# Kernel optimization log

Hardware: AMD Instinct MI355X
Metric: run time of the kernel (lower is better)

The kernel has to match this reference:

```python
import jax, jax.numpy as jnp
import numpy as np

D = 1024
F = 256
EPS = 1e-5


def layer_norm(x, g, b):
    mu = jnp.mean(x, axis=-1, keepdims=True)
    var = jnp.mean((x - mu) ** 2, axis=-1, keepdims=True)
    return (x - mu) * jax.lax.rsqrt(var + EPS) * g + b


def setup_inputs() -> dict:
    key = jax.random.key(0)
    ks = jax.random.split(key, 8)
    B, S = 4, 4096
    return {
        "bottom_up_input": jax.random.normal(ks[0], (B, S, D), dtype=jnp.float32),
        "top_down_prediction": jax.random.normal(ks[1], (B, S, D), dtype=jnp.float32),
        "W_spec": jax.random.normal(ks[2], (2 * F, D), dtype=jnp.float32) * 0.02,
        "log_decay": jnp.linspace(-3.0, -0.001, F, dtype=jnp.float32),
        "frequencies": jax.random.normal(ks[3], (F,), dtype=jnp.float32) * 0.1,
        "W_from": jax.random.normal(ks[4], (D, 2 * F), dtype=jnp.float32) * 0.02,
        "ln1_g": jnp.ones((D,), jnp.float32),
        "ln1_b": jnp.zeros((D,), jnp.float32),
        "W1": jax.random.normal(ks[5], (D, D), dtype=jnp.float32) * 0.02,
        "b1": jnp.zeros((D,), jnp.float32),
        "W2": jax.random.normal(ks[6], (D, D), dtype=jnp.float32) * 0.02,
        "b2": jnp.zeros((D,), jnp.float32),
        "ln2_g": jnp.ones((D,), jnp.float32),
        "ln2_b": jnp.zeros((D,), jnp.float32),
        "error_weight": jnp.asarray(0.1, jnp.float32),
    }


def spectral_conv(x, W_spec, log_decay, frequencies, W_from, ln1_g, ln1_b):
    # x: [B,S,D]
    x = layer_norm(x, ln1_g, ln1_b)
    B, S, _ = x.shape
    spectral = jnp.einsum('bsd,fd->bsf', x, W_spec)  # [B,S,2F]
    u = jax.lax.complex(spectral[..., :F], spectral[..., F:])  # [B,S,F] complex
    decay = jax.nn.sigmoid(log_decay)
    omega = jnp.tanh(frequencies) * 0.1  # dt = 1.0
    rot = jax.lax.complex(jnp.cos(omega), jnp.sin(omega))  # [F]
    A = (decay * rot).astype(jnp.complex64)  # [F]
    # kernel[t] = A^t * rot, built with cumprod as in the original
    ones = jnp.ones((1, F), dtype=A.dtype)
    A_seq = jnp.broadcast_to(A[None, :], (S - 1, F))
    powers = jnp.cumprod(jnp.concatenate([ones, A_seq], axis=0), axis=0)  # [S,F]
    kernel = (powers * rot[None, :])[None]  # [1,S,F]
    n_fft = 2 * S
    U_f = jnp.fft.fft(u, n=n_fft, axis=1)
    K_f = jnp.fft.fft(kernel, n=n_fft, axis=1)
    y = jnp.fft.ifft(U_f * K_f, n=n_fft, axis=1)[:, :S, :]  # [B,S,F]
    spectral_out = jnp.concatenate([y.real, y.imag], axis=-1)  # [B,S,2F]
    return jnp.einsum('bsf,df->bsd', spectral_out, W_from)


def reference(bottom_up_input, top_down_prediction, W_spec, log_decay, frequencies,
              W_from, ln1_g, ln1_b, W1, b1, W2, b2, ln2_g, ln2_b, error_weight):
    bu_repr = spectral_conv(bottom_up_input, W_spec, log_decay, frequencies,
                            W_from, ln1_g, ln1_b)
    error = jnp.clip(bu_repr - top_down_prediction, -1.0, 1.0)
    corrected = bu_repr - jax.nn.sigmoid(error_weight) * error
    prediction_error = jnp.clip(jnp.mean(error ** 2), 0.0, 1.0)
    h = jax.nn.gelu(jnp.einsum('bsd,ed->bse', corrected, W1) + b1, approximate=False)
    h = jnp.einsum('bsd,ed->bse', h, W2) + b2
    next_prediction = layer_norm(h, ln2_g, ln2_b)
    return corrected, next_prediction, prediction_error
```

## Files before the change

kernel.cpp:

```cpp
#include <hip/hip_runtime.h>
#include <math.h>

#define Dn 1024
#define Fn 256
#define Sn 4096
#define Bn 4
#define Mn (Bn*Sn)
#define CHn 256
#define NCn (Sn/CHn)

typedef __bf16 bf16x8 __attribute__((ext_vector_type(8)));
typedef float  f32x4  __attribute__((ext_vector_type(4)));

__device__ inline unsigned short f2bf(float f) {
  unsigned int u = __float_as_uint(f);
  u += 0x7fffu + ((u >> 16) & 1u);
  return (unsigned short)(u >> 16);
}
__device__ inline float bf2f(unsigned short s) {
  return __uint_as_float(((unsigned int)s) << 16);
}

__device__ inline void async16(const void* g, void* l) {
  __builtin_amdgcn_global_load_lds(
      (__attribute__((address_space(1))) void*)(g),
      (__attribute__((address_space(3))) void*)(l), 16, 0, 0);
}

#define WAITVM(n) __builtin_amdgcn_s_waitcnt(0xF70 | (n))
#define BARRIER() asm volatile("s_barrier" ::: "memory")

__global__ __launch_bounds__(256) void convert_weights(
    const float* __restrict__ wspec, const float* __restrict__ wfrom,
    const float* __restrict__ w1, const float* __restrict__ w2,
    unsigned short* __restrict__ o_spec, unsigned short* __restrict__ o_from,
    unsigned short* __restrict__ o_w1, unsigned short* __restrict__ o_w2) {
  int i = blockIdx.x * 256 + threadIdx.x;
  if (i < 524288) {
    o_spec[i] = f2bf(wspec[i]);
    o_from[i] = f2bf(wfrom[i]);
  }
  o_w1[i] = f2bf(w1[i]);
  o_w2[i] = f2bf(w2[i]);
}

template <int OUT_BF16>
__global__ __launch_bounds__(256) void ln_kernel(
    const float* __restrict__ x, const float* __restrict__ g,
    const float* __restrict__ b, void* __restrict__ out) {
  int row = blockIdx.x, tid = threadIdx.x;
  int wid = tid >> 6, lane = tid & 63;
  float4 v = ((const float4*)(x + (size_t)row * Dn))[tid];
  float s  = v.x + v.y + v.z + v.w;
  float ss = v.x * v.x + v.y * v.y + v.z * v.z + v.w * v.w;
  #pragma unroll
  for (int o = 32; o; o >>= 1) {
    s  += __shfl_down(s, o);
    ss += __shfl_down(ss, o);
  }
  __shared__ float r1[4], r2[4];
  if (lane == 0) { r1[wid] = s; r2[wid] = ss; }
  __syncthreads();
  s  = r1[0] + r1[1] + r1[2] + r1[3];
  ss = r2[0] + r2[1] + r2[2] + r2[3];
  float mu  = s * (1.0f / Dn);
  float var = ss * (1.0f / Dn) - mu * mu;
  float rs  = rsqrtf(var + 1e-5f);
  float4 gv = ((const float4*)g)[tid];
  float4 bv = ((const float4*)b)[tid];
  float o0 = (v.x - mu) * rs * gv.x + bv.x;
  float o1 = (v.y - mu) * rs * gv.y + bv.y;
  float o2 = (v.z - mu) * rs * gv.z + bv.z;
  float o3 = (v.w - mu) * rs * gv.w + bv.w;
  if (OUT_BF16) {
    ushort4 w;
    w.x = f2bf(o0); w.y = f2bf(o1); w.z = f2bf(o2); w.w = f2bf(o3);
    ((ushort4*)out)[(size_t)row * 256 + tid] = w;
  } else {
    float4 w; w.x = o0; w.y = o1; w.z = o2; w.w = o3;
    ((float4*)out)[(size_t)row * 256 + tid] = w;
  }
}

template <int MODE>
__global__ __launch_bounds__(256) void gemm_bt(
    const unsigned short* __restrict__ A, const unsigned short* __restrict__ Bw,
    int K, int N,
    float* __restrict__ outF, unsigned short* __restrict__ outH,
    const float* __restrict__ td, const float* __restrict__ bias,
    const float* __restrict__ ew, float* __restrict__ errAcc) {
  __shared__ unsigned short As[3 * 4096];
  __shared__ unsigned short Bs[3 * 4096];
  __shared__ float red[4];

  int tid = threadIdx.x;
  int wid = tid >> 6, lane = tid & 63;
  int wm = wid >> 1, wn = wid & 1;
  int quad = lane >> 4, l16 = lane & 15;

  int g = blockIdx.x + gridDim.x * blockIdx.y;
  int nbn = gridDim.x;
  int gh = g >> 3;
  int bn = gh % nbn;
  int bm = (g & 7) + (gh / nbn) * 8;

  int r_lo = lane >> 2;
  int c8   = (lane & 3) * 8;

  const unsigned short* Abase = A + (size_t)bm * 128 * K;
  const unsigned short* Bbase = Bw + (size_t)bn * 128 * K;

  f32x4 acc[4][4] = {};

  const int T = K >> 5;
  auto issue = [&](int t, int stg) {
    int k0 = t << 5;
    #pragma unroll
    for (int s = 0; s < 2; ++s) {
      int chunk = s * 4 + wid;
      int r = chunk * 16 + r_lo;
      async16(Abase + (size_t)r * K + k0 + c8, As + stg * 4096 + chunk * 512);
      async16(Bbase + (size_t)r * K + k0 + c8, Bs + stg * 4096 + chunk * 512);
    }
  };

  issue(0, 0);
  if (T > 1) issue(1, 1);

  int stg = 0, stg2 = 2;
  for (int k = 0; k < T; ++k) {
    if (k + 1 < T) WAITVM(4); else WAITVM(0);
    BARRIER();
    if (k + 2 < T) issue(k + 2, stg2);

    const unsigned short* Ab = As + stg * 4096;
    const unsigned short* Bb = Bs + stg * 4096;
    bf16x8 af[4], bf[4];
    #pragma unroll
    for (int i = 0; i < 4; i++)
      af[i] = *(const bf16x8*)(Ab + (wm * 64 + i * 16 + l16) * 32 + quad * 8);
    #pragma unroll
    for (int j = 0; j < 4; j++)
      bf[j] = *(const bf16x8*)(Bb + (wn * 64 + j * 16 + l16) * 32 + quad * 8);
    #pragma unroll
    for (int i = 0; i < 4; i++)
      #pragma unroll
      for (int j = 0; j < 4; j++)
        acc[i][j] = __builtin_amdgcn_mfma_f32_16x16x32_bf16(af[i], bf[j], acc[i][j], 0, 0, 0);

    stg  = (stg  == 2) ? 0 : stg  + 1;
    stg2 = (stg2 == 2) ? 0 : stg2 + 1;
  }

  float esum = 0.0f;
  float sigw = 0.0f;
  if (MODE == 1) sigw = 1.0f / (1.0f + expf(-ew[0]));

  #pragma unroll
  for (int i = 0; i < 4; i++) {
    int row_base = bm * 128 + wm * 64 + i * 16 + quad * 4;
    #pragma unroll
    for (int j = 0; j < 4; j++) {
      int col = bn * 128 + wn * 64 + j * 16 + l16;
      #pragma unroll
      for (int r = 0; r < 4; r++) {
        size_t idx = (size_t)(row_base + r) * N + col;
        float v = acc[i][j][r];
        if (MODE == 0) {
          outH[idx] = f2bf(v);
        } else if (MODE == 1) {
          float e = v - td[idx];
          e = fminf(fmaxf(e, -1.0f), 1.0f);
          float corr = v - sigw * e;
          outF[idx] = corr;
          outH[idx] = f2bf(corr);
          esum += e * e;
        } else if (MODE == 2) {
          float h = v + bias[col];
          float gel = 0.5f * h * (1.0f + erff(h * 0.70710678118654752f));
          outH[idx] = f2bf(gel);
        } else {
          outF[idx] = v + bias[col];
        }
      }
    }
  }

  if (MODE == 1) {
    #pragma unroll
    for (int o = 32; o; o >>= 1) esum += __shfl_down(esum, o);
    if (lane == 0) red[wid] = esum;
    __syncthreads();
    if (tid == 0) atomicAdd(errAcc, red[0] + red[1] + red[2] + red[3]);
  }
}

__global__ __launch_bounds__(256) void scan_partial(
    const unsigned short* __restrict__ spec, const float* __restrict__ log_decay,
    const float* __restrict__ freq, float2* __restrict__ chunkfin) {
  int f = threadIdx.x;
  int bx = blockIdx.x;
  int b = bx / NCn, c = bx % NCn;
  float dec = 1.0f / (1.0f + expf(-log_decay[f]));
  float om  = tanhf(freq[f]) * 0.1f;
  float Are = dec * cosf(om), Aim = dec * sinf(om);
  const unsigned short* u = spec + ((size_t)b * Sn + (size_t)c * CHn) * 512 + f;
  float sre = 0.0f, sim = 0.0f;
  for (int t = 0; t < CHn; t++) {
    float ure = bf2f(u[(size_t)t * 512]);
    float uim = bf2f(u[(size_t)t * 512 + 256]);
    float nre = Are * sre - Aim * sim + ure;
    float nim = Are * sim + Aim * sre + uim;
    sre = nre; sim = nim;
  }
  chunkfin[(size_t)bx * 256 + f] = make_float2(sre, sim);
}

__global__ __launch_bounds__(256) void scan_carry(
    const float* __restrict__ log_decay, const float* __restrict__ freq,
    const float2* __restrict__ chunkfin, float2* __restrict__ carries) {
  int f = threadIdx.x;
  int b = blockIdx.x;
  float dec = 1.0f / (1.0f + expf(-log_decay[f]));
  float om  = tanhf(freq[f]) * 0.1f;
  float pre = dec * cosf(om), pim = dec * sinf(om);
  #pragma unroll
  for (int i = 0; i < 8; i++) {
    float nr = pre * pre - pim * pim;
    float ni = 2.0f * pre * pim;
    pre = nr; pim = ni;
  }
  float sre = 0.0f, sim = 0.0f;
  for (int c = 0; c < NCn; c++) {
    carries[(size_t)(b * NCn + c) * 256 + f] = make_float2(sre, sim);
    float2 cf = chunkfin[(size_t)(b * NCn + c) * 256 + f];
    float nre = pre * sre - pim * sim + cf.x;
    float nim = pre * sim + pim * sre + cf.y;
    sre = nre; sim = nim;
  }
}

__global__ __launch_bounds__(256) void scan_final(
    const unsigned short* __restrict__ spec, const float* __restrict__ log_decay,
    const float* __restrict__ freq, const float2* __restrict__ carries,
    unsigned short* __restrict__ outH) {
  int f = threadIdx.x;
  int bx = blockIdx.x;
  int b = bx / NCn, c = bx % NCn;
  float dec = 1.0f / (1.0f + expf(-log_decay[f]));
  float om  = tanhf(freq[f]) * 0.1f;
  float Are = dec * cosf(om), Aim = dec * sinf(om);
  float Rre = cosf(om), Rim = sinf(om);
  float2 s0 = carries[(size_t)bx * 256 + f];
  float sre = s0.x, sim = s0.y;
  const unsigned short* u = spec + ((size_t)b * Sn + (size_t)c * CHn) * 512 + f;
  unsigned short* o = outH + ((size_t)b * Sn + (size_t)c * CHn) * 512 + f;
  for (int t = 0; t < CHn; t++) {
    float ure = bf2f(u[(size_t)t * 512]);
    float uim = bf2f(u[(size_t)t * 512 + 256]);
    float nre = Are * sre - Aim * sim + ure;
    float nim = Are * sim + Aim * sre + uim;
    sre = nre; sim = nim;
    o[(size_t)t * 512]       = f2bf(Rre * sre - Rim * sim);
    o[(size_t)t * 512 + 256] = f2bf(Rre * sim + Rim * sre);
  }
}

__global__ void finalize_err(const float* __restrict__ errAcc, float* __restrict__ out) {
  float m = errAcc[0] * (1.0f / 16777216.0f);
  out[0] = fminf(fmaxf(m, 0.0f), 1.0f);
}

extern "C" void kernel_launch(void* const* d_in, const int* in_sizes, int n_in,
                              void* d_out, int out_size, void* d_ws, size_t ws_size,
                              hipStream_t stream) {
  (void)in_sizes; (void)n_in; (void)out_size; (void)ws_size;
  const float* x     = (const float*)d_in[0];
  const float* td    = (const float*)d_in[1];
  const float* wspec = (const float*)d_in[2];
  const float* logd  = (const float*)d_in[3];
  const float* freq  = (const float*)d_in[4];
  const float* wfrom = (const float*)d_in[5];
  const float* g1    = (const float*)d_in[6];
  const float* b1ln  = (const float*)d_in[7];
  const float* W1    = (const float*)d_in[8];
  const float* b1    = (const float*)d_in[9];
  const float* W2    = (const float*)d_in[10];
  const float* b2    = (const float*)d_in[11];
  const float* g2    = (const float*)d_in[12];
  const float* b2ln  = (const float*)d_in[13];
  const float* ew    = (const float*)d_in[14];

  char* ws = (char*)d_ws;
  size_t off = 0;
  float* errAcc = (float*)(ws + off);              off += 256;
  unsigned short* wspec_h = (unsigned short*)(ws + off); off += (size_t)512 * 1024 * 2;
  unsigned short* wfrom_h = (unsigned short*)(ws + off); off += (size_t)1024 * 512 * 2;
  unsigned short* w1_h    = (unsigned short*)(ws + off); off += (size_t)1024 * 1024 * 2;
  unsigned short* w2_h    = (unsigned short*)(ws + off); off += (size_t)1024 * 1024 * 2;
  unsigned short* xn_h   = (unsigned short*)(ws + off);
  unsigned short* corr_h = (unsigned short*)(ws + off); off += (size_t)Mn * 1024 * 2;
  unsigned short* spec  = (unsigned short*)(ws + off);
  unsigned short* h1_h  = (unsigned short*)(ws + off);  off += (size_t)Mn * 1024 * 2;
  unsigned short* so_h = (unsigned short*)(ws + off);  off += (size_t)Mn * 512 * 2;
  float2* chunkfin = (float2*)(ws + off);              off += (size_t)Bn * NCn * 256 * 8;
  float2* carries  = (float2*)(ws + off);              off += (size_t)Bn * NCn * 256 * 8;

  float* outCorr = (float*)d_out;
  float* outNP   = outCorr + (size_t)Mn * 1024;
  float* outErr  = outNP + (size_t)Mn * 1024;

  hipMemsetAsync(errAcc, 0, 4, stream);
  convert_weights<<<4096, 256, 0, stream>>>(wspec, wfrom, W1, W2,
                                            wspec_h, wfrom_h, w1_h, w2_h);
  ln_kernel<1><<<Mn, 256, 0, stream>>>(x, g1, b1ln, xn_h);
  gemm_bt<0><<<dim3(512 / 128, Mn / 128), 256, 0, stream>>>(
      xn_h, wspec_h, 1024, 512, nullptr, spec, nullptr, nullptr, nullptr, nullptr);
  scan_partial<<<Bn * NCn, 256, 0, stream>>>(spec, logd, freq, chunkfin);
  scan_carry<<<Bn, 256, 0, stream>>>(logd, freq, chunkfin, carries);
  scan_final<<<Bn * NCn, 256, 0, stream>>>(spec, logd, freq, carries, so_h);
  gemm_bt<1><<<dim3(1024 / 128, Mn / 128), 256, 0, stream>>>(
      so_h, wfrom_h, 512, 1024, outCorr, corr_h, td, nullptr, ew, errAcc);
  gemm_bt<2><<<dim3(1024 / 128, Mn / 128), 256, 0, stream>>>(
      corr_h, w1_h, 1024, 1024, nullptr, h1_h, nullptr, b1, nullptr, nullptr);
  gemm_bt<3><<<dim3(1024 / 128, Mn / 128), 256, 0, stream>>>(
      h1_h, w2_h, 1024, 1024, outNP, nullptr, nullptr, b2, nullptr, nullptr);
  ln_kernel<0><<<Mn, 256, 0, stream>>>(outNP, g2, b2ln, outNP);
  finalize_err<<<1, 1, 0, stream>>>(errAcc, outErr);
}
```

Measured before the change: 512.4 us.

## Use double-buffered GEMM with occupancy hint and bf16 intermediate before final LayerNorm

The GEMM pipeline goes from triple to double buffering of shared memory, and it now waits for all loads before each tile instead of keeping two tiles in flight. A launch-bounds occupancy hint of 4 blocks per CU is added. The last GEMM writes its bias-added output as bf16 to scratch, and the final LayerNorm reads that bf16 input instead of an fp32 round trip through the output buffer. This cuts LDS use and memory traffic but reduces load/compute overlap and loses some precision before the LayerNorm.

Measured after the change: 480.6 us. 1.07x faster.

```diff
diff --git a/kernel.cpp b/kernel.cpp
--- a/kernel.cpp
+++ b/kernel.cpp
@@ -44,13 +44,19 @@
   o_w2[i] = f2bf(w2[i]);
 }
 
-template <int OUT_BF16>
+template <int IN_BF16, int OUT_BF16>
 __global__ __launch_bounds__(256) void ln_kernel(
-    const float* __restrict__ x, const float* __restrict__ g,
+    const void* __restrict__ xin, const float* __restrict__ g,
     const float* __restrict__ b, void* __restrict__ out) {
   int row = blockIdx.x, tid = threadIdx.x;
   int wid = tid >> 6, lane = tid & 63;
-  float4 v = ((const float4*)(x + (size_t)row * Dn))[tid];
+  float4 v;
+  if (IN_BF16) {
+    ushort4 u = ((const ushort4*)xin)[(size_t)row * 256 + tid];
+    v.x = bf2f(u.x); v.y = bf2f(u.y); v.z = bf2f(u.z); v.w = bf2f(u.w);
+  } else {
+    v = ((const float4*)xin)[(size_t)row * 256 + tid];
+  }
   float s  = v.x + v.y + v.z + v.w;
   float ss = v.x * v.x + v.y * v.y + v.z * v.z + v.w * v.w;
   #pragma unroll
@@ -83,14 +89,14 @@
 }
 
 template <int MODE>
-__global__ __launch_bounds__(256) void gemm_bt(
+__global__ __launch_bounds__(256, 4) void gemm_bt(
     const unsigned short* __restrict__ A, const unsigned short* __restrict__ Bw,
     int K, int N,
     float* __restrict__ outF, unsigned short* __restrict__ outH,
     const float* __restrict__ td, const float* __restrict__ bias,
     const float* __restrict__ ew, float* __restrict__ errAcc) {
-  __shared__ unsigned short As[3 * 4096];
-  __shared__ unsigned short Bs[3 * 4096];
+  __shared__ unsigned short As[2 * 4096];
+  __shared__ unsigned short Bs[2 * 4096];
   __shared__ float red[4];
 
   int tid = threadIdx.x;
@@ -125,16 +131,14 @@
   };
 
   issue(0, 0);
-  if (T > 1) issue(1, 1);
-
-  int stg = 0, stg2 = 2;
+
   for (int k = 0; k < T; ++k) {
-    if (k + 1 < T) WAITVM(4); else WAITVM(0);
+    WAITVM(0);
     BARRIER();
-    if (k + 2 < T) issue(k + 2, stg2);
-
-    const unsigned short* Ab = As + stg * 4096;
-    const unsigned short* Bb = Bs + stg * 4096;
+    if (k + 1 < T) issue(k + 1, (k + 1) & 1);
+
+    const unsigned short* Ab = As + (k & 1) * 4096;
+    const unsigned short* Bb = Bs + (k & 1) * 4096;
     bf16x8 af[4], bf[4];
     #pragma unroll
     for (int i = 0; i < 4; i++)
@@ -147,9 +151,6 @@
       #pragma unroll
       for (int j = 0; j < 4; j++)
         acc[i][j] = __builtin_amdgcn_mfma_f32_16x16x32_bf16(af[i], bf[j], acc[i][j], 0, 0, 0);
-
-    stg  = (stg  == 2) ? 0 : stg  + 1;
-    stg2 = (stg2 == 2) ? 0 : stg2 + 1;
   }
 
   float esum = 0.0f;
@@ -179,8 +180,10 @@
           float h = v + bias[col];
           float gel = 0.5f * h * (1.0f + erff(h * 0.70710678118654752f));
           outH[idx] = f2bf(gel);
+        } else if (MODE == 3) {
+          outF[idx] = v + bias[col];
         } else {
-          outF[idx] = v + bias[col];
+          outH[idx] = f2bf(v + bias[col]);
         }
       }
     }
@@ -299,7 +302,8 @@
   unsigned short* w1_h    = (unsigned short*)(ws + off); off += (size_t)1024 * 1024 * 2;
   unsigned short* w2_h    = (unsigned short*)(ws + off); off += (size_t)1024 * 1024 * 2;
   unsigned short* xn_h   = (unsigned short*)(ws + off);
-  unsigned short* corr_h = (unsigned short*)(ws + off); off += (size_t)Mn * 1024 * 2;
+  unsigned short* corr_h = (unsigned short*)(ws + off);
+  unsigned short* h2_h   = (unsigned short*)(ws + off); off += (size_t)Mn * 1024 * 2;
   unsigned short* spec  = (unsigned short*)(ws + off);
   unsigned short* h1_h  = (unsigned short*)(ws + off);  off += (size_t)Mn * 1024 * 2;
   unsigned short* so_h = (unsigned short*)(ws + off);  off += (size_t)Mn * 512 * 2;
@@ -313,7 +317,7 @@
   hipMemsetAsync(errAcc, 0, 4, stream);
   convert_weights<<<4096, 256, 0, stream>>>(wspec, wfrom, W1, W2,
                                             wspec_h, wfrom_h, w1_h, w2_h);
-  ln_kernel<1><<<Mn, 256, 0, stream>>>(x, g1, b1ln, xn_h);
+  ln_kernel<0, 1><<<Mn, 256, 0, stream>>>(x, g1, b1ln, xn_h);
   gemm_bt<0><<<dim3(512 / 128, Mn / 128), 256, 0, stream>>>(
       xn_h, wspec_h, 1024, 512, nullptr, spec, nullptr, nullptr, nullptr, nullptr);
   scan_partial<<<Bn * NCn, 256, 0, stream>>>(spec, logd, freq, chunkfin);
@@ -323,8 +327,8 @@
       so_h, wfrom_h, 512, 1024, outCorr, corr_h, td, nullptr, ew, errAcc);
   gemm_bt<2><<<dim3(1024 / 128, Mn / 128), 256, 0, stream>>>(
       corr_h, w1_h, 1024, 1024, nullptr, h1_h, nullptr, b1, nullptr, nullptr);
-  gemm_bt<3><<<dim3(1024 / 128, Mn / 128), 256, 0, stream>>>(
-      h1_h, w2_h, 1024, 1024, outNP, nullptr, nullptr, b2, nullptr, nullptr);
-  ln_kernel<0><<<Mn, 256, 0, stream>>>(outNP, g2, b2ln, outNP);
+  gemm_bt<4><<<dim3(1024 / 128, Mn / 128), 256, 0, stream>>>(
+      h1_h, w2_h, 1024, 1024, nullptr, h2_h, nullptr, b2, nullptr, nullptr);
+  ln_kernel<1, 0><<<Mn, 256, 0, stream>>>(h2_h, g2, b2ln, outNP);
   finalize_err<<<1, 1, 0, stream>>>(errAcc, outErr);
 }
```
